# Performance work log

Measured on AMD Instinct MI355X. Metric: run time of the kernel, lower is better.

The kernel has to match this reference:

```python
import jax, jax.numpy as jnp
import numpy as np

K = 7            # kernel_size
PAD = K // 2
B, C, H, W = 16, 4, 128, 128   # in_channels == out_channels == 4


def setup_inputs() -> dict:
    key = jax.random.key(0)
    kx, kw = jax.random.split(key)
    x = jax.random.normal(kx, (B, C, H, W), dtype=jnp.float32)
    # nn.Parameter init: randn * 0.0001 / kernel_size
    weight = jax.random.normal(kw, (1, C, C, H, W, K * K), dtype=jnp.float32) * (0.0001 / K)
    return {"x": x, "weight": weight}


def reference(x, weight):
    # fmri mask computed on the (possibly) pre-padded input
    mask = (x != 0).astype(x.dtype)                       # (B,C,H,W)
    xp = jnp.pad(x, ((0, 0), (0, 0), (PAD, PAD), (PAD, PAD)))
    # unfold(2,K,1).unfold(3,K,1).view(..., K*K): taps ordered row-major (dy, dx)
    patches = jnp.stack(
        [xp[:, :, dy:dy + H, dx:dx + W] for dy in range(K) for dx in range(K)],
        axis=-1,
    )                                                      # (B,C,H,W,K*K)
    # weight_bias: delta kernel (1 at the center tap)
    wb = jnp.zeros((1, C, C, H, W, K * K), dtype=x.dtype).at[..., (K * K) // 2].set(1.0)
    cw = weight + wb
    # L1-normalized absolute weights over the tap dimension
    wn = jnp.abs(cw) / jnp.sum(jnp.abs(cw), axis=-1, keepdims=True)
    # out[b,o,h,w] = sum_{i,t} patches[b,i,h,w,t] * wn[0,o,i,h,w,t]
    out = jnp.einsum('bihwt,oihwt->bohw', patches, wn[0])
    return out * mask
```

## Files before the change

kernel.cpp:

```cpp
#include <hip/hip_runtime.h>


#define HW   128
#define PW   134
#define NB   16
#define NC   4
#define KK   49

__global__ __launch_bounds__(256) void lc2d_prep(const float* __restrict__ x,
                                                 float* __restrict__ xTp) {
  int idx = blockIdx.x * 256 + threadIdx.x;
  if (idx >= NC * PW * PW) return;
  int wp = idx % PW;
  int r  = idx / PW;
  int hp = r % PW;
  int i  = r / PW;
  int h = hp - 3, w = wp - 3;
  bool in = (h >= 0) & (h < HW) & (w >= 0) & (w < HW);
  float v[NB];
#pragma unroll
  for (int b = 0; b < NB; ++b)
    v[b] = in ? x[((b * NC + i) * HW + h) * HW + w] : 0.0f;
  float4* dst = (float4*)(xTp + (size_t)idx * NB);
  dst[0] = make_float4(v[0],  v[1],  v[2],  v[3]);
  dst[1] = make_float4(v[4],  v[5],  v[6],  v[7]);
  dst[2] = make_float4(v[8],  v[9],  v[10], v[11]);
  dst[3] = make_float4(v[12], v[13], v[14], v[15]);
}

template <int MODE>
__global__ __launch_bounds__(256) void lc2d_main(const float* __restrict__ weight,
                                                 const float* __restrict__ xsrc,
                                                 float* __restrict__ out) {
  const int tid = threadIdx.x;
  const int b   = tid & 15;
  const int pos = tid >> 4;
  const int wc  = blockIdx.x & 7;
  const int h   = blockIdx.x >> 3;
  const int w0  = wc * 16;
  const int w   = w0 + pos;

  __shared__ __align__(16) float Wl[NC][16][60];
  __shared__ float Inv[NC][16];

  float acc[NC] = {0.f, 0.f, 0.f, 0.f};

  for (int i = 0; i < NC; ++i) {
    __syncthreads();
    const int base = (i * 16384 + h * HW + w0) * KK;
#pragma unroll
    for (int k = 0; k < 13; ++k) {
      int f = tid + k * 256;
      if (f < 3136) {
        int o  = f / 784;
        int r  = f - o * 784;
        int ps = r / 49;
        int ts = r - ps * 49;
        int dy = ts / 7;
        int dx = ts - dy * 7;
        Wl[o][ps][dy * 8 + dx] = weight[base + o * 3211264 + r];
      }
    }
    __syncthreads();
    if (tid < 64) {
      int o = tid >> 4, ps = tid & 15;
      float s = 0.f;
#pragma unroll
      for (int dy = 0; dy < 7; ++dy) {
        float4 qa = *(const float4*)&Wl[o][ps][dy * 8];
        float4 qb = *(const float4*)&Wl[o][ps][dy * 8 + 4];
        s += fabsf(qa.x) + fabsf(qa.y) + fabsf(qa.z) + fabsf(qa.w)
           + fabsf(qb.x) + fabsf(qb.y) + fabsf(qb.z);
      }
      float v = Wl[o][ps][27];
      s += fabsf(v + 1.f) - fabsf(v);
      Inv[o][ps] = 1.f / s;
    }
    __syncthreads();
#pragma unroll
    for (int k = 0; k < 13; ++k) {
      int f = tid + k * 256;
      if (f < 3136) {
        int o  = f / 784;
        int r  = f - o * 784;
        int ps = r / 49;
        int ts = r - ps * 49;
        int dy = ts / 7;
        int dx = ts - dy * 7;
        float v = Wl[o][ps][dy * 8 + dx];
        if (ts == 24) v += 1.f;
        Wl[o][ps][dy * 8 + dx] = fabsf(v) * Inv[o][ps];
      }
    }
    __syncthreads();
    float xv[7];
#pragma unroll
    for (int dy = 0; dy < 7; ++dy) {
      if (MODE == 0) {
        const float* xr = xsrc + ((size_t)((i * PW + h + dy) * PW + w) * NB + b);
#pragma unroll
        for (int dx = 0; dx < 7; ++dx) xv[dx] = xr[dx * NB];
      } else {
        int hh = h + dy - 3;
        bool hin = (hh >= 0) & (hh < HW);
#pragma unroll
        for (int dx = 0; dx < 7; ++dx) {
          int ww = w + dx - 3;
          bool in = hin & (ww >= 0) & (ww < HW);
          xv[dx] = in ? xsrc[((b * NC + i) * HW + hh) * HW + ww] : 0.f;
        }
      }
#pragma unroll
      for (int o = 0; o < NC; ++o) {
        float4 qa = *(const float4*)&Wl[o][pos][dy * 8];
        float4 qb = *(const float4*)&Wl[o][pos][dy * 8 + 4];
        acc[o] = fmaf(xv[0], qa.x, acc[o]);
        acc[o] = fmaf(xv[1], qa.y, acc[o]);
        acc[o] = fmaf(xv[2], qa.z, acc[o]);
        acc[o] = fmaf(xv[3], qa.w, acc[o]);
        acc[o] = fmaf(xv[4], qb.x, acc[o]);
        acc[o] = fmaf(xv[5], qb.y, acc[o]);
        acc[o] = fmaf(xv[6], qb.z, acc[o]);
      }
    }
  }
#pragma unroll
  for (int o = 0; o < NC; ++o) {
    float xc;
    if (MODE == 0)
      xc = xsrc[(size_t)((o * PW + (h + 3)) * PW + (w + 3)) * NB + b];
    else
      xc = xsrc[((b * NC + o) * HW + h) * HW + w];
    out[((b * NC + o) * HW + h) * HW + w] = (xc != 0.f) ? acc[o] : 0.f;
  }
}

extern "C" void kernel_launch(void* const* d_in, const int* in_sizes, int n_in,
                              void* d_out, int out_size, void* d_ws, size_t ws_size,
                              hipStream_t stream) {
  const float* x      = (const float*)d_in[0];
  const float* weight = (const float*)d_in[1];
  float* out = (float*)d_out;

  const size_t xtp_bytes = (size_t)NC * PW * PW * NB * sizeof(float);
  if (ws_size >= xtp_bytes) {
    float* xTp = (float*)d_ws;
    lc2d_prep<<<(NC * PW * PW + 255) / 256, 256, 0, stream>>>(x, xTp);
    lc2d_main<0><<<1024, 256, 0, stream>>>(weight, xTp, out);
  } else {
    lc2d_main<1><<<1024, 256, 0, stream>>>(weight, x, out);
  }
}
```

Measured before the change: 135.9 us.

## Split input channels across blocks with atomic accumulation and vectorized weight loads

Each block now handles one input channel instead of looping over all four, so the grid grows from 1024 to 4096 blocks and partial sums are combined with atomicAdd into an output that is zeroed first with a memset. Weights are loaded as contiguous float4 into an unpadded shared panel, and the L1 normalization runs across all threads using shuffle reductions instead of 64 threads. The aim is more parallelism, fewer barriers and better-coalesced reads of the large weight tensor. The cost is an extra memset, four atomic adds per output element, and possible bank conflicts from the 49-float stride in shared memory.

```diff
diff --git a/kernel.cpp b/kernel.cpp
--- a/kernel.cpp
+++ b/kernel.cpp
@@ -1,11 +1,14 @@
 #include <hip/hip_runtime.h>
 
 
-#define HW   128
-#define PW   134
-#define NB   16
-#define NC   4
-#define KK   49
+#define HW 128
+#define PW 134
+#define NB 16
+#define NC 4
+#define KK 49
+#define PANEL 784
+#define OSTRIDE 3211264
+#define ISTRIDE 802816
 
 __global__ __launch_bounds__(256) void lc2d_prep(const float* __restrict__ x,
                                                  float* __restrict__ xTp) {
@@ -32,98 +35,83 @@
 __global__ __launch_bounds__(256) void lc2d_main(const float* __restrict__ weight,
                                                  const float* __restrict__ xsrc,
                                                  float* __restrict__ out) {
+  __shared__ __align__(16) float Raw[NC * PANEL];
+
   const int tid = threadIdx.x;
+  const int bid = blockIdx.x;
+  const int i   = bid >> 10;
+  const int r2  = bid & 1023;
+  const int h   = r2 >> 3;
+  const int wc  = r2 & 7;
+  const int w0  = wc * 16;
+
+  const size_t wbase = (size_t)i * ISTRIDE + (size_t)(h * HW + w0) * KK;
+#pragma unroll
+  for (int k = 0; k < 4; ++k) {
+    int f = tid + k * 256;
+    if (f < 784) {
+      int o = f / 196;
+      int g = f - o * 196;
+      float4 v = *(const float4*)(weight + wbase + (size_t)o * OSTRIDE + 4 * g);
+      *(float4*)(&Raw[o * PANEL + 4 * g]) = v;
+    }
+  }
+  __syncthreads();
+
+  {
+    const int r    = tid >> 2;
+    const int q    = tid & 3;
+    const int rowb = (r >> 4) * PANEL + (r & 15) * KK;
+    const int t0   = q * 12;
+    float v[13];
+#pragma unroll
+    for (int j = 0; j < 12; ++j) v[j] = Raw[rowb + t0 + j];
+    v[12] = (q == 3) ? Raw[rowb + 48] : 0.f;
+    float s = 0.f;
+#pragma unroll
+    for (int j = 0; j < 13; ++j) s += fabsf(v[j]);
+    if (q == 2) s += fabsf(v[0] + 1.f) - fabsf(v[0]);
+    s += __shfl_xor(s, 1);
+    s += __shfl_xor(s, 2);
+    const float inv = 1.f / s;
+    if (q == 2) v[0] += 1.f;
+#pragma unroll
+    for (int j = 0; j < 12; ++j) Raw[rowb + t0 + j] = fabsf(v[j]) * inv;
+    if (q == 3) Raw[rowb + 48] = fabsf(v[12]) * inv;
+  }
+  __syncthreads();
+
   const int b   = tid & 15;
   const int pos = tid >> 4;
-  const int wc  = blockIdx.x & 7;
-  const int h   = blockIdx.x >> 3;
-  const int w0  = wc * 16;
   const int w   = w0 + pos;
-
-  __shared__ __align__(16) float Wl[NC][16][60];
-  __shared__ float Inv[NC][16];
-
   float acc[NC] = {0.f, 0.f, 0.f, 0.f};
 
-  for (int i = 0; i < NC; ++i) {
-    __syncthreads();
-    const int base = (i * 16384 + h * HW + w0) * KK;
+  float xv[7];
 #pragma unroll
-    for (int k = 0; k < 13; ++k) {
-      int f = tid + k * 256;
-      if (f < 3136) {
-        int o  = f / 784;
-        int r  = f - o * 784;
-        int ps = r / 49;
-        int ts = r - ps * 49;
-        int dy = ts / 7;
-        int dx = ts - dy * 7;
-        Wl[o][ps][dy * 8 + dx] = weight[base + o * 3211264 + r];
+  for (int dy = 0; dy < 7; ++dy) {
+    if (MODE == 0) {
+      const float* xr = xsrc + ((size_t)((i * PW + h + dy) * PW + w) * NB + b);
+#pragma unroll
+      for (int dx = 0; dx < 7; ++dx) xv[dx] = xr[dx * NB];
+    } else {
+      int hh = h + dy - 3;
+      bool hin = (hh >= 0) & (hh < HW);
+#pragma unroll
+      for (int dx = 0; dx < 7; ++dx) {
+        int ww = w + dx - 3;
+        bool in = hin & (ww >= 0) & (ww < HW);
+        xv[dx] = in ? xsrc[((b * NC + i) * HW + hh) * HW + ww] : 0.f;
       }
     }
-    __syncthreads();
-    if (tid < 64) {
-      int o = tid >> 4, ps = tid & 15;
-      float s = 0.f;
 #pragma unroll
-      for (int dy = 0; dy < 7; ++dy) {
-        float4 qa = *(const float4*)&Wl[o][ps][dy * 8];
-        float4 qb = *(const float4*)&Wl[o][ps][dy * 8 + 4];
-        s += fabsf(qa.x) + fabsf(qa.y) + fabsf(qa.z) + fabsf(qa.w)
-           + fabsf(qb.x) + fabsf(qb.y) + fabsf(qb.z);
-      }
-      float v = Wl[o][ps][27];
-      s += fabsf(v + 1.f) - fabsf(v);
-      Inv[o][ps] = 1.f / s;
-    }
-    __syncthreads();
+    for (int o = 0; o < NC; ++o) {
+      const float* wr = &Raw[o * PANEL + pos * KK + dy * 7];
 #pragma unroll
-    for (int k = 0; k < 13; ++k) {
-      int f = tid + k * 256;
-      if (f < 3136) {
-        int o  = f / 784;
-        int r  = f - o * 784;
-        int ps = r / 49;
-        int ts = r - ps * 49;
-        int dy = ts / 7;
-        int dx = ts - dy * 7;
-        float v = Wl[o][ps][dy * 8 + dx];
-        if (ts == 24) v += 1.f;
-        Wl[o][ps][dy * 8 + dx] = fabsf(v) * Inv[o][ps];
-      }
-    }
-    __syncthreads();
-    float xv[7];
-#pragma unroll
-    for (int dy = 0; dy < 7; ++dy) {
-      if (MODE == 0) {
-        const float* xr = xsrc + ((size_t)((i * PW + h + dy) * PW + w) * NB + b);
-#pragma unroll
-        for (int dx = 0; dx < 7; ++dx) xv[dx] = xr[dx * NB];
-      } else {
-        int hh = h + dy - 3;
-        bool hin = (hh >= 0) & (hh < HW);
-#pragma unroll
-        for (int dx = 0; dx < 7; ++dx) {
-          int ww = w + dx - 3;
-          bool in = hin & (ww >= 0) & (ww < HW);
-          xv[dx] = in ? xsrc[((b * NC + i) * HW + hh) * HW + ww] : 0.f;
-        }
-      }
-#pragma unroll
-      for (int o = 0; o < NC; ++o) {
-        float4 qa = *(const float4*)&Wl[o][pos][dy * 8];
-        float4 qb = *(const float4*)&Wl[o][pos][dy * 8 + 4];
-        acc[o] = fmaf(xv[0], qa.x, acc[o]);
-        acc[o] = fmaf(xv[1], qa.y, acc[o]);
-        acc[o] = fmaf(xv[2], qa.z, acc[o]);
-        acc[o] = fmaf(xv[3], qa.w, acc[o]);
-        acc[o] = fmaf(xv[4], qb.x, acc[o]);
-        acc[o] = fmaf(xv[5], qb.y, acc[o]);
-        acc[o] = fmaf(xv[6], qb.z, acc[o]);
-      }
+      for (int dx = 0; dx < 7; ++dx)
+        acc[o] = fmaf(xv[dx], wr[dx], acc[o]);
     }
   }
+
 #pragma unroll
   for (int o = 0; o < NC; ++o) {
     float xc;
@@ -131,7 +119,7 @@
       xc = xsrc[(size_t)((o * PW + (h + 3)) * PW + (w + 3)) * NB + b];
     else
       xc = xsrc[((b * NC + o) * HW + h) * HW + w];
-    out[((b * NC + o) * HW + h) * HW + w] = (xc != 0.f) ? acc[o] : 0.f;
+    atomicAdd(&out[((b * NC + o) * HW + h) * HW + w], (xc != 0.f) ? acc[o] : 0.f);
   }
 }
 
@@ -142,12 +130,14 @@
   const float* weight = (const float*)d_in[1];
   float* out = (float*)d_out;
 
+  hipMemsetAsync(d_out, 0, (size_t)out_size * sizeof(float), stream);
+
   const size_t xtp_bytes = (size_t)NC * PW * PW * NB * sizeof(float);
   if (ws_size >= xtp_bytes) {
     float* xTp = (float*)d_ws;
     lc2d_prep<<<(NC * PW * PW + 255) / 256, 256, 0, stream>>>(x, xTp);
-    lc2d_main<0><<<1024, 256, 0, stream>>>(weight, xTp, out);
+    lc2d_main<0><<<4096, 256, 0, stream>>>(weight, xTp, out);
   } else {
-    lc2d_main<1><<<1024, 256, 0, stream>>>(weight, x, out);
+    lc2d_main<1><<<4096, 256, 0, stream>>>(weight, x, out);
   }
 }
```

Result: slower. 150.7 us (+10.9%).
